# Kernel tuning notes

Hardware: AMD Instinct MI355X
Metric: run time of the kernel (lower is better)

Reference implementation:

```python
import jax, jax.numpy as jnp
import numpy as np

D_MODEL = 1024
NUM_HEADS = 16
D_K = D_MODEL // NUM_HEADS
NEG_INF = -1e9


def setup_inputs() -> dict:
    key = jax.random.key(0)
    ks = jax.random.split(key, 12)
    B, N_IMG, L_Q = 32, 576, 256
    img = jax.random.normal(ks[0], (B, N_IMG, D_MODEL), dtype=jnp.float32)
    que = jax.random.normal(ks[1], (B, L_Q, D_MODEL), dtype=jnp.float32)
    mask_img = jax.random.randint(ks[2], (B, N_IMG), 0, 2, dtype=jnp.int32)
    mask_que = jax.random.randint(ks[3], (B, L_Q), 0, 2, dtype=jnp.int32)
    s = 0.02  # init scale keeps scores in a sane range
    Wi = jax.random.normal(ks[4], (3, D_MODEL, D_MODEL), dtype=jnp.float32) * s
    bi = jax.random.normal(ks[5], (3, D_MODEL), dtype=jnp.float32) * s
    Wq = jax.random.normal(ks[6], (3, D_MODEL, D_MODEL), dtype=jnp.float32) * s
    bq = jax.random.normal(ks[7], (3, D_MODEL), dtype=jnp.float32) * s
    Wp = jax.random.normal(ks[8], (2, D_MODEL, D_MODEL), dtype=jnp.float32) * s
    bp = jax.random.normal(ks[9], (2, D_MODEL), dtype=jnp.float32) * s
    return {"img": img, "que": que, "Wi": Wi, "bi": bi, "Wq": Wq, "bq": bq,
            "Wp": Wp, "bp": bp, "mask_img": mask_img, "mask_que": mask_que}


def _proj_heads(x, W, b):
    # torch Linear: x @ W.T + b, then [B, L, H, d_k] -> [B, H, L, d_k]
    B, L, _ = x.shape
    out = jnp.einsum("bld,ed->ble", x, W) + b
    return out.reshape(B, L, NUM_HEADS, D_K).transpose(0, 2, 1, 3)


def _attention(q, k, v, mask_key):
    # q: [B,H,Lq,dk], k/v: [B,H,Lk,dk], mask_key: [B,Lk] (0 = masked)
    scores = jnp.einsum("bhqd,bhkd->bhqk", q, k) / jnp.sqrt(jnp.asarray(D_K, q.dtype))
    scores = jnp.where(mask_key[:, None, None, :] == 0, NEG_INF, scores)
    p = jax.nn.softmax(scores, axis=-1)
    attn = jnp.einsum("bhqk,bhkd->bhqd", p, v)
    B, H, Lq, dk = attn.shape
    return attn.transpose(0, 2, 1, 3).reshape(B, Lq, H * dk)


def reference(img, que, Wi, bi, Wq, bq, Wp, bp, mask_img, mask_que):
    iq = _proj_heads(img, Wi[0], bi[0])
    ik = _proj_heads(img, Wi[1], bi[1])
    iv = _proj_heads(img, Wi[2], bi[2])
    qq = _proj_heads(que, Wq[0], bq[0])
    qk = _proj_heads(que, Wq[1], bq[1])
    qv = _proj_heads(que, Wq[2], bq[2])
    q2i = _attention(iq, qk, qv, mask_que)  # [B, N_img, d_model]
    i2q = _attention(qq, ik, iv, mask_img)  # [B, L_q, d_model]
    out0 = jnp.einsum("bld,ed->ble", q2i, Wp[0]) + bp[0]
    out1 = jnp.einsum("bld,ed->ble", i2q, Wp[1]) + bp[1]
    return (out0, out1)
```

## Files before the change

### kernel.cpp

```cpp
#include <hip/hip_runtime.h>


typedef __bf16 bf16;
typedef __attribute__((ext_vector_type(8))) __bf16 bf16x8;
typedef __attribute__((ext_vector_type(4))) __bf16 bf16x4;
typedef __attribute__((ext_vector_type(2))) __bf16 bf16x2;
typedef __attribute__((ext_vector_type(4))) float f32x4;

__device__ __forceinline__ void g2lds16(const void* g, void* l) {
  __builtin_amdgcn_global_load_lds((const __attribute__((address_space(1))) void*)g,
                                   (__attribute__((address_space(3))) void*)l,
                                   16, 0, 0);
}

__global__ void cvt_bf16_multi(const float* s0, bf16* d0, int n0,
                               const float* s1, bf16* d1, int n1,
                               const float* s2, bf16* d2, int n2,
                               const float* s3, bf16* d3, int n3,
                               const float* s4, bf16* d4, int n4c) {
  const int total = n0 + n1 + n2 + n3 + n4c;
  const int stride = gridDim.x * blockDim.x;
  for (int i = blockIdx.x * blockDim.x + threadIdx.x; i < total; i += stride) {
    int j = i;
    const float* s; bf16* d;
    if (j < n0) { s = s0; d = d0; }
    else { j -= n0;
      if (j < n1) { s = s1; d = d1; }
      else { j -= n1;
        if (j < n2) { s = s2; d = d2; }
        else { j -= n2;
          if (j < n3) { s = s3; d = d3; }
          else { j -= n3; s = s4; d = d4; }
        }
      }
    }
    const float4 v = ((const float4*)s)[j];
    bf16x4 o = {(bf16)v.x, (bf16)v.y, (bf16)v.z, (bf16)v.w};
    ((bf16x4*)d)[j] = o;
  }
}

template <int MODE>
__global__ __launch_bounds__(256, 2)
void gemm_bt(const bf16* __restrict__ A, const bf16* __restrict__ Bw,
             const float* __restrict__ bias, void* __restrict__ outp, int Lrow) {
  __shared__ alignas(16) bf16 As[128 * 64];
  __shared__ alignas(16) bf16 Bs[128 * 64];
  const int tid = threadIdx.x;
  const int w = tid >> 6, lane = tid & 63;
  const int lr = lane & 15, quad = lane >> 4;
  const int i_q4 = quad * 4;
  const int mBase = blockIdx.y * 128, nBase = blockIdx.x * 128;
  const int wr = (w >> 1) * 64, wc = (w & 1) * 64;

  const int swl = (((lane & 7) ^ ((lane >> 3) & 7)) * 8);
  const bf16* Ab = A + (size_t)(mBase + (lane >> 3)) * 1024 + swl;
  const bf16* Bb = Bw + (size_t)(nBase + (lane >> 3)) * 1024 + swl;

  f32x4 acc[4][4] = {};
  for (int kt = 0; kt < 16; ++kt) {
    const int k0 = kt * 64;
#pragma unroll
    for (int c = 0; c < 4; ++c) {
      const int rowOff = w * 32 + c * 8;
      g2lds16(Ab + (size_t)rowOff * 1024 + k0, As + rowOff * 64);
      g2lds16(Bb + (size_t)rowOff * 1024 + k0, Bs + rowOff * 64);
    }
    __syncthreads();
#pragma unroll
    for (int kk = 0; kk < 64; kk += 32) {
      const int sOff = ((quad | (kk >> 3)) ^ (lr & 7)) * 8;
      bf16x8 a[4], b[4];
#pragma unroll
      for (int i = 0; i < 4; ++i)
        a[i] = *(const bf16x8*)(As + (wr + i * 16 + lr) * 64 + sOff);
#pragma unroll
      for (int j = 0; j < 4; ++j)
        b[j] = *(const bf16x8*)(Bs + (wc + j * 16 + lr) * 64 + sOff);
#pragma unroll
      for (int i = 0; i < 4; ++i)
#pragma unroll
        for (int j = 0; j < 4; ++j)
          acc[i][j] = __builtin_amdgcn_mfma_f32_16x16x32_bf16(a[i], b[j], acc[i][j], 0, 0, 0);
    }
    __syncthreads();
  }

  if constexpr (MODE == 1) {
    float* out = (float*)outp;
#pragma unroll
    for (int j = 0; j < 4; ++j) {
      const int e = nBase + wc + j * 16 + lr;
      const float bv = bias[e];
#pragma unroll
      for (int i = 0; i < 4; ++i) {
        const int mb = mBase + wr + i * 16 + i_q4;
#pragma unroll
        for (int r = 0; r < 4; ++r)
          out[(size_t)(mb + r) * 1024 + e] = acc[i][j][r] + bv;
      }
    }
  } else {
    bf16* out = (bf16*)outp;
    const int L = Lrow;
    const size_t slab = (size_t)512 * L * 64;
    int bb[4], ll[4];
#pragma unroll
    for (int i = 0; i < 4; ++i) {
      const int m = mBase + wr + i * 16 + i_q4;
      bb[i] = m / L;
      ll[i] = m - bb[i] * L;
    }
#pragma unroll
    for (int j = 0; j < 4; ++j) {
      const int eb = nBase + wc + j * 16;
      const int p = eb >> 10, h = (eb >> 6) & 15, d = (eb & 63) + lr;
      const float bv = bias[eb + lr];
      if (p < 2) {
        bf16* o2 = out + (size_t)p * slab;
#pragma unroll
        for (int i = 0; i < 4; ++i) {
          bf16* o3 = o2 + ((size_t)(bb[i] * 16 + h) * L + ll[i]) * 64 + d;
#pragma unroll
          for (int r = 0; r < 4; ++r) o3[r * 64] = (bf16)(acc[i][j][r] + bv);
        }
      } else {
        bf16* o2 = out + 2 * slab;
#pragma unroll
        for (int i = 0; i < 4; ++i) {
          bf16x4 v;
#pragma unroll
          for (int r = 0; r < 4; ++r) v[r] = (bf16)(acc[i][j][r] + bv);
          *(bf16x4*)(o2 + ((size_t)(bb[i] * 16 + h) * 64 + d) * L + ll[i]) = v;
        }
      }
    }
  }
}

#define PSTR 40
__global__ __launch_bounds__(256)
void attn(const bf16* __restrict__ Q, const bf16* __restrict__ K,
          const bf16* __restrict__ Vt, const int* __restrict__ mask,
          bf16* __restrict__ out, int Lq, int Lk) {
  __shared__ float mk[576];
  __shared__ alignas(16) bf16 pb[4][2][2][16 * PSTR];
  const int tid = threadIdx.x;
  const int w = tid >> 6, lane = tid & 63;
  const int lr = lane & 15, quad = lane >> 4, i_q4 = quad * 4;
  const int bh = blockIdx.y, b = bh >> 4, h = bh & 15;
  const int q0 = blockIdx.x * 128 + w * 32;

  for (int k = tid; k < Lk; k += 256)
    mk[k] = (mask[b * Lk + k] == 0) ? -1e9f : 0.0f;
  __syncthreads();
  if (q0 >= Lq) return;

  bf16x8 qa[2][2];
#pragma unroll
  for (int i = 0; i < 2; ++i) {
    const bf16* Qb = Q + ((size_t)bh * Lq + q0 + i * 16 + lr) * 64 + quad * 8;
    qa[i][0] = *(const bf16x8*)(Qb);
    qa[i][1] = *(const bf16x8*)(Qb + 32);
  }
  const bf16* Kb = K + (size_t)bh * Lk * 64;
  const bf16* Vb = Vt + (size_t)bh * 64 * Lk;

  bf16x8 kc[2][2], kn[2][2], vc[4], vn[4];
  {
    const bf16* kp = Kb + (size_t)(lr * 2) * 64 + quad * 8;
    kc[0][0] = *(const bf16x8*)(kp);       kc[0][1] = *(const bf16x8*)(kp + 32);
    kc[1][0] = *(const bf16x8*)(kp + 64);  kc[1][1] = *(const bf16x8*)(kp + 96);
    const bf16* vp = Vb + quad * 8;
#pragma unroll
    for (int j = 0; j < 4; ++j) vc[j] = *(const bf16x8*)(vp + (size_t)(j * 16 + lr) * Lk);
  }

  f32x4 o[2][4] = {};
  float ls[2][4] = {};
  const int nkt = Lk >> 5;
  constexpr float SCL = 0.18033688f;
#pragma unroll 2
  for (int kt = 0; kt < nkt; ++kt) {
    const int kp1 = (kt + 1 < nkt) ? kt + 1 : kt;
    {
      const bf16* kp = Kb + ((size_t)kp1 * 32 + lr * 2) * 64 + quad * 8;
      kn[0][0] = *(const bf16x8*)(kp);       kn[0][1] = *(const bf16x8*)(kp + 32);
      kn[1][0] = *(const bf16x8*)(kp + 64);  kn[1][1] = *(const bf16x8*)(kp + 96);
      const bf16* vp = Vb + kp1 * 32 + quad * 8;
#pragma unroll
      for (int j = 0; j < 4; ++j) vn[j] = *(const bf16x8*)(vp + (size_t)(j * 16 + lr) * Lk);
    }

    f32x4 c[2][2];
#pragma unroll
    for (int i = 0; i < 2; ++i)
#pragma unroll
      for (int jn = 0; jn < 2; ++jn) {
        const f32x4 z = {};
        c[i][jn] = __builtin_amdgcn_mfma_f32_16x16x32_bf16(qa[i][0], kc[jn][0], z, 0, 0, 0);
        c[i][jn] = __builtin_amdgcn_mfma_f32_16x16x32_bf16(qa[i][1], kc[jn][1], c[i][jn], 0, 0, 0);
      }

    const float m0 = mk[kt * 32 + lr * 2], m1 = mk[kt * 32 + lr * 2 + 1];
#pragma unroll
    for (int i = 0; i < 2; ++i) {
      bf16* pw = &pb[w][kt & 1][i][0];
#pragma unroll
      for (int r = 0; r < 4; ++r) {
        const float p0 = __builtin_amdgcn_exp2f(__builtin_fmaf(c[i][0][r], SCL, m0));
        const float p1 = __builtin_amdgcn_exp2f(__builtin_fmaf(c[i][1][r], SCL, m1));
        ls[i][r] += p0 + p1;
        bf16x2 pp = {(bf16)p0, (bf16)p1};
        *(bf16x2*)(pw + (i_q4 + r) * PSTR + lr * 2) = pp;
      }
    }
#pragma unroll
    for (int i = 0; i < 2; ++i) {
      const bf16x8 pa = *(const bf16x8*)(&pb[w][kt & 1][i][0] + lr * PSTR + quad * 8);
#pragma unroll
      for (int j = 0; j < 4; ++j)
        o[i][j] = __builtin_amdgcn_mfma_f32_16x16x32_bf16(pa, vc[j], o[i][j], 0, 0, 0);
    }
#pragma unroll
    for (int jn = 0; jn < 2; ++jn)
#pragma unroll
      for (int kh = 0; kh < 2; ++kh) kc[jn][kh] = kn[jn][kh];
#pragma unroll
    for (int j = 0; j < 4; ++j) vc[j] = vn[j];
  }

  float inv[2][4];
#pragma unroll
  for (int i = 0; i < 2; ++i)
#pragma unroll
    for (int r = 0; r < 4; ++r) {
      float s = ls[i][r];
#pragma unroll
      for (int off = 1; off < 16; off <<= 1) s += __shfl_xor(s, off);
      inv[i][r] = 1.0f / s;
    }

#pragma unroll
  for (int i = 0; i < 2; ++i) {
    bf16* ob = out + ((size_t)b * Lq + q0 + i * 16 + i_q4) * 1024 + h * 64;
#pragma unroll
    for (int j = 0; j < 4; ++j)
#pragma unroll
      for (int r = 0; r < 4; ++r)
        ob[(size_t)r * 1024 + j * 16 + lr] = (bf16)(o[i][j][r] * inv[i][r]);
  }
}

extern "C" void kernel_launch(void* const* d_in, const int* in_sizes, int n_in,
                              void* d_out, int out_size, void* d_ws, size_t ws_size,
                              hipStream_t stream) {
  const float* img = (const float*)d_in[0];
  const float* que = (const float*)d_in[1];
  const float* Wi  = (const float*)d_in[2];
  const float* bi  = (const float*)d_in[3];
  const float* Wq  = (const float*)d_in[4];
  const float* bq  = (const float*)d_in[5];
  const float* Wp  = (const float*)d_in[6];
  const float* bp  = (const float*)d_in[7];
  const int* mimg = (const int*)d_in[8];
  const int* mque = (const int*)d_in[9];
  float* out = (float*)d_out;

  bf16* X1  = (bf16*)d_ws;
  bf16* X2  = X1 + 18874368;
  bf16* WiB = X2 + 8388608;
  bf16* WqB = WiB + 3145728;
  bf16* WpB = WqB + 3145728;
  bf16* PI  = WpB + 2097152;
  bf16* PQ  = PI + 56623104;

  cvt_bf16_multi<<<8192, 256, 0, stream>>>(img, X1, 18874368 / 4,
                                           que, X2, 8388608 / 4,
                                           Wi, WiB, 3145728 / 4,
                                           Wq, WqB, 3145728 / 4,
                                           Wp, WpB, 2097152 / 4);

  gemm_bt<0><<<dim3(24, 144), 256, 0, stream>>>(X1, WiB, bi, PI, 576);
  gemm_bt<0><<<dim3(24, 64), 256, 0, stream>>>(X2, WqB, bq, PQ, 256);

  const size_t SI = 18874368, SQ = 8388608;
  attn<<<dim3(5, 512), 256, 0, stream>>>(PI, PQ + SQ, PQ + 2 * SQ, mque, X1, 576, 256);
  attn<<<dim3(2, 512), 256, 0, stream>>>(PQ, PI + SI, PI + 2 * SI, mimg, X2, 256, 576);

  gemm_bt<1><<<dim3(8, 144), 256, 0, stream>>>(X1, WpB, bp, out, 0);
  gemm_bt<1><<<dim3(8, 64), 256, 0, stream>>>(X2, WpB + 1048576, bp + 1024, out + 18874368, 0);
}
```

Measured before the change: 642.1 us.

## Triple-buffer GEMM LDS loads with 256x128 tiles and 512-thread blocks

The projection and output GEMMs now use 256x128 output tiles computed by eight waves. Global-to-LDS loads run through a three-stage ring buffer: tile t+2 is prefetched while tile t is computed, and explicit vmcnt waits plus barriers replace the two per-iteration __syncthreads. MFMA sections are wrapped in s_setprio to favour math issue. This aims to hide global load latency and cut barrier stalls, at the cost of about 147KB of LDS per block, which limits occupancy to one block per CU.

After: 753.7 us. +17.4%, slower.

```diff
diff --git a/kernel.cpp b/kernel.cpp
--- a/kernel.cpp
+++ b/kernel.cpp
@@ -41,49 +41,75 @@
 }
 
 template <int MODE>
-__global__ __launch_bounds__(256, 2)
+__global__ __launch_bounds__(512, 2)
 void gemm_bt(const bf16* __restrict__ A, const bf16* __restrict__ Bw,
              const float* __restrict__ bias, void* __restrict__ outp, int Lrow) {
-  __shared__ alignas(16) bf16 As[128 * 64];
-  __shared__ alignas(16) bf16 Bs[128 * 64];
+  __shared__ alignas(16) bf16 As[3][256 * 64];
+  __shared__ alignas(16) bf16 Bs[3][128 * 64];
   const int tid = threadIdx.x;
   const int w = tid >> 6, lane = tid & 63;
   const int lr = lane & 15, quad = lane >> 4;
   const int i_q4 = quad * 4;
-  const int mBase = blockIdx.y * 128, nBase = blockIdx.x * 128;
+  const int mBase = blockIdx.y * 256, nBase = blockIdx.x * 128;
   const int wr = (w >> 1) * 64, wc = (w & 1) * 64;
 
   const int swl = (((lane & 7) ^ ((lane >> 3) & 7)) * 8);
   const bf16* Ab = A + (size_t)(mBase + (lane >> 3)) * 1024 + swl;
   const bf16* Bb = Bw + (size_t)(nBase + (lane >> 3)) * 1024 + swl;
 
+  auto STAGE = [&](int kt, int s) {
+    const int k0 = kt * 64;
+#pragma unroll
+    for (int c = 0; c < 4; ++c) {
+      const int r = w * 32 + c * 8;
+      g2lds16(Ab + (size_t)r * 1024 + k0, &As[s][r * 64]);
+    }
+#pragma unroll
+    for (int c = 0; c < 2; ++c) {
+      const int r = w * 16 + c * 8;
+      g2lds16(Bb + (size_t)r * 1024 + k0, &Bs[s][r * 64]);
+    }
+  };
+
   f32x4 acc[4][4] = {};
-  for (int kt = 0; kt < 16; ++kt) {
-    const int k0 = kt * 64;
-#pragma unroll
-    for (int c = 0; c < 4; ++c) {
-      const int rowOff = w * 32 + c * 8;
-      g2lds16(Ab + (size_t)rowOff * 1024 + k0, As + rowOff * 64);
-      g2lds16(Bb + (size_t)rowOff * 1024 + k0, Bs + rowOff * 64);
-    }
-    __syncthreads();
-#pragma unroll
-    for (int kk = 0; kk < 64; kk += 32) {
-      const int sOff = ((quad | (kk >> 3)) ^ (lr & 7)) * 8;
-      bf16x8 a[4], b[4];
+
+  STAGE(0, 0);
+  STAGE(1, 1);
+  asm volatile("s_waitcnt vmcnt(6)" ::: "memory");
+  __builtin_amdgcn_s_barrier();
+
+  int s0 = 0;
+  for (int t = 0; t < 16; ++t) {
+    const int s2 = (s0 >= 1) ? s0 - 1 : s0 + 2;
+    if (t + 2 < 16) STAGE(t + 2, s2);
+    bf16x8 a[2][4], b[2][4];
+#pragma unroll
+    for (int ks = 0; ks < 2; ++ks) {
+      const int sOff = ((quad | (ks << 2)) ^ (lr & 7)) * 8;
+      const bf16* Ar = &As[s0][(wr + lr) * 64 + sOff];
+      const bf16* Br = &Bs[s0][(wc + lr) * 64 + sOff];
+#pragma unroll
+      for (int i = 0; i < 4; ++i) a[ks][i] = *(const bf16x8*)(Ar + i * 1024);
+#pragma unroll
+      for (int j = 0; j < 4; ++j) b[ks][j] = *(const bf16x8*)(Br + j * 1024);
+    }
+    __builtin_amdgcn_s_setprio(1);
+#pragma unroll
+    for (int ks = 0; ks < 2; ++ks)
 #pragma unroll
       for (int i = 0; i < 4; ++i)
-        a[i] = *(const bf16x8*)(As + (wr + i * 16 + lr) * 64 + sOff);
-#pragma unroll
-      for (int j = 0; j < 4; ++j)
-        b[j] = *(const bf16x8*)(Bs + (wc + j * 16 + lr) * 64 + sOff);
-#pragma unroll
-      for (int i = 0; i < 4; ++i)
 #pragma unroll
         for (int j = 0; j < 4; ++j)
-          acc[i][j] = __builtin_amdgcn_mfma_f32_16x16x32_bf16(a[i], b[j], acc[i][j], 0, 0, 0);
-    }
-    __syncthreads();
+          acc[i][j] = __builtin_amdgcn_mfma_f32_16x16x32_bf16(a[ks][i], b[ks][j], acc[i][j], 0, 0, 0);
+    __builtin_amdgcn_s_setprio(0);
+    if (t < 14) {
+      asm volatile("s_waitcnt vmcnt(6)" ::: "memory");
+      __builtin_amdgcn_s_barrier();
+    } else if (t == 14) {
+      asm volatile("s_waitcnt vmcnt(0)" ::: "memory");
+      __builtin_amdgcn_s_barrier();
+    }
+    s0 = (s0 < 2) ? s0 + 1 : 0;
   }
 
   if constexpr (MODE == 1) {
@@ -281,13 +307,13 @@
                                            Wq, WqB, 3145728 / 4,
                                            Wp, WpB, 2097152 / 4);
 
-  gemm_bt<0><<<dim3(24, 144), 256, 0, stream>>>(X1, WiB, bi, PI, 576);
-  gemm_bt<0><<<dim3(24, 64), 256, 0, stream>>>(X2, WqB, bq, PQ, 256);
+  gemm_bt<0><<<dim3(24, 72), 512, 0, stream>>>(X1, WiB, bi, PI, 576);
+  gemm_bt<0><<<dim3(24, 32), 512, 0, stream>>>(X2, WqB, bq, PQ, 256);
 
   const size_t SI = 18874368, SQ = 8388608;
   attn<<<dim3(5, 512), 256, 0, stream>>>(PI, PQ + SQ, PQ + 2 * SQ, mque, X1, 576, 256);
   attn<<<dim3(2, 512), 256, 0, stream>>>(PQ, PI + SI, PI + 2 * SI, mimg, X2, 256, 576);
 
-  gemm_bt<1><<<dim3(8, 144), 256, 0, stream>>>(X1, WpB, bp, out, 0);
-  gemm_bt<1><<<dim3(8, 64), 256, 0, stream>>>(X2, WpB + 1048576, bp + 1024, out + 18874368, 0);
-}
+  gemm_bt<1><<<dim3(8, 72), 512, 0, stream>>>(X1, WpB, bp, out, 0);
+  gemm_bt<1><<<dim3(8, 32), 512, 0, stream>>>(X2, WpB + 1048576, bp + 1024, out + 18874368, 0);
+}
```

## Merge paired GEMM and attention launches into single grids with XCD-aware block remap

Applied to the files above, without the earlier changes.

The img and que projection GEMMs, the two attention directions, and the two output GEMMs are each fused into one launch that picks its operand set from the block index. The GEMM blocks are also remapped so consecutive row tiles land on the same XCD, which should improve L2 reuse of the shared A and W tiles. This removes three launches and the tail idle time between back-to-back small grids. The cost is a little extra index arithmetic and branch setup per block.

After: 661.4 us. +3.0%, slower.

```diff
diff --git a/kernel.cpp b/kernel.cpp
--- a/kernel.cpp
+++ b/kernel.cpp
@@ -42,15 +42,30 @@
 
 template <int MODE>
 __global__ __launch_bounds__(256, 2)
-void gemm_bt(const bf16* __restrict__ A, const bf16* __restrict__ Bw,
-             const float* __restrict__ bias, void* __restrict__ outp, int Lrow) {
+void gemm_bt(const bf16* __restrict__ A0, const bf16* __restrict__ W0,
+             const float* __restrict__ bi0, void* __restrict__ o0, int L0,
+             const bf16* __restrict__ A1, const bf16* __restrict__ W1,
+             const float* __restrict__ bi1, void* __restrict__ o1, int L1,
+             int ySplit) {
   __shared__ alignas(16) bf16 As[128 * 64];
   __shared__ alignas(16) bf16 Bs[128 * 64];
   const int tid = threadIdx.x;
   const int w = tid >> 6, lane = tid & 63;
   const int lr = lane & 15, quad = lane >> 4;
   const int i_q4 = quad * 4;
-  const int mBase = blockIdx.y * 128, nBase = blockIdx.x * 128;
+
+  const int nx = (int)gridDim.x;
+  const int lid = (int)blockIdx.y * nx + (int)blockIdx.x;
+  const int xcd = lid & 7, s = lid >> 3;
+  const int ry = (int)gridDim.y >> 3;
+  const int sy = s / nx;
+  const int vx = s - sy * nx;
+  int vy = xcd * ry + sy;
+
+  const bf16* A; const bf16* Bw; const float* bias; void* outp; int Lrow;
+  if (vy < ySplit) { A = A0; Bw = W0; bias = bi0; outp = o0; Lrow = L0; }
+  else { vy -= ySplit; A = A1; Bw = W1; bias = bi1; outp = o1; Lrow = L1; }
+  const int mBase = vy * 128, nBase = vx * 128;
   const int wr = (w >> 1) * 64, wc = (w & 1) * 64;
 
   const int swl = (((lane & 7) ^ ((lane >> 3) & 7)) * 8);
@@ -140,16 +155,24 @@
 
 #define PSTR 40
 __global__ __launch_bounds__(256)
-void attn(const bf16* __restrict__ Q, const bf16* __restrict__ K,
-          const bf16* __restrict__ Vt, const int* __restrict__ mask,
-          bf16* __restrict__ out, int Lq, int Lk) {
+void attn(const bf16* __restrict__ Q0, const bf16* __restrict__ K0,
+          const bf16* __restrict__ V0, const int* __restrict__ mk0,
+          bf16* __restrict__ ou0, int Lq0, int Lk0, int xSplit,
+          const bf16* __restrict__ Q1, const bf16* __restrict__ K1,
+          const bf16* __restrict__ V1, const int* __restrict__ mk1,
+          bf16* __restrict__ ou1, int Lq1, int Lk1) {
   __shared__ float mk[576];
   __shared__ alignas(16) bf16 pb[4][2][2][16 * PSTR];
   const int tid = threadIdx.x;
   const int w = tid >> 6, lane = tid & 63;
   const int lr = lane & 15, quad = lane >> 4, i_q4 = quad * 4;
   const int bh = blockIdx.y, b = bh >> 4, h = bh & 15;
-  const int q0 = blockIdx.x * 128 + w * 32;
+
+  const bf16* Q; const bf16* K; const bf16* Vt; const int* mask; bf16* out;
+  int Lq, Lk, gx = (int)blockIdx.x;
+  if (gx < xSplit) { Q = Q0; K = K0; Vt = V0; mask = mk0; out = ou0; Lq = Lq0; Lk = Lk0; }
+  else { gx -= xSplit; Q = Q1; K = K1; Vt = V1; mask = mk1; out = ou1; Lq = Lq1; Lk = Lk1; }
+  const int q0 = gx * 128 + w * 32;
 
   for (int k = tid; k < Lk; k += 256)
     mk[k] = (mask[b * Lk + k] == 0) ? -1e9f : 0.0f;
@@ -281,13 +304,13 @@
                                            Wq, WqB, 3145728 / 4,
                                            Wp, WpB, 2097152 / 4);
 
-  gemm_bt<0><<<dim3(24, 144), 256, 0, stream>>>(X1, WiB, bi, PI, 576);
-  gemm_bt<0><<<dim3(24, 64), 256, 0, stream>>>(X2, WqB, bq, PQ, 256);
+  gemm_bt<0><<<dim3(24, 208), 256, 0, stream>>>(X1, WiB, bi, PI, 576,
+                                                X2, WqB, bq, PQ, 256, 144);
 
   const size_t SI = 18874368, SQ = 8388608;
-  attn<<<dim3(5, 512), 256, 0, stream>>>(PI, PQ + SQ, PQ + 2 * SQ, mque, X1, 576, 256);
-  attn<<<dim3(2, 512), 256, 0, stream>>>(PQ, PI + SI, PI + 2 * SI, mimg, X2, 256, 576);
-
-  gemm_bt<1><<<dim3(8, 144), 256, 0, stream>>>(X1, WpB, bp, out, 0);
-  gemm_bt<1><<<dim3(8, 64), 256, 0, stream>>>(X2, WpB + 1048576, bp + 1024, out + 18874368, 0);
-}
+  attn<<<dim3(7, 512), 256, 0, stream>>>(PI, PQ + SQ, PQ + 2 * SQ, mque, X1, 576, 256, 5,
+                                         PQ, PI + SI, PI + 2 * SI, mimg, X2, 256, 576);
+
+  gemm_bt<1><<<dim3(8, 208), 256, 0, stream>>>(X1, WpB, bp, out, 0,
+                                               X2, WpB + 1048576, bp + 1024, out + 18874368, 0, 144);
+}
```
